# Optimization experiments

Measured on AMD Instinct MI355X. Metric: run time of the kernel, lower is better.

Reference implementation:

```python
import jax, jax.numpy as jnp
import numpy as np

H = 64          # index_n_heads
D = 128         # index_head_dim (== FP8 quant block size -> one scale per row)
RD = 64         # qk_rope_head_dim
TOPK = 512      # index_topk
THETA = 10000.0
SM_SCALE = D ** -0.5


def _fwht(x):
    """Sylvester-ordered fast Walsh-Hadamard transform over last dim, scaled by d^-0.5."""
    d = x.shape[-1]
    orig = x.shape
    y = x.reshape(-1, d)
    m = 1
    while m < d:  # static loop, log2(d)=7 iters
        y = y.reshape(-1, d // (2 * m), 2, m)
        a, b = y[:, :, 0, :], y[:, :, 1, :]
        y = jnp.stack([a + b, a - b], axis=2)
        m *= 2
    return y.reshape(orig) * (d ** -0.5)


def _interleaved_to_half(x):
    # [..., d] with (even, odd) interleaving -> [evens..., odds...]
    return jnp.concatenate([x[..., 0::2], x[..., 1::2]], axis=-1)


def _rope_half(x, cos, sin):
    # x: [..., RD] in half format; cos/sin broadcastable to [..., RD//2]
    x1, x2 = x[..., : RD // 2], x[..., RD // 2:]
    return jnp.concatenate([x1 * cos - x2 * sin, x2 * cos + x1 * sin], axis=-1)


def _layernorm(x, g, b, eps=1e-5):
    mu = jnp.mean(x, axis=-1, keepdims=True)
    var = jnp.mean(jnp.square(x - mu), axis=-1, keepdims=True)
    return (x - mu) * jax.lax.rsqrt(var + eps) * g + b


def _fp8_ue8m0_quant(x2d):
    """Per-row FP8 e4m3 quantization with UE8M0 (power-of-two) scales. x2d: (M, 128)."""
    amax = jnp.maximum(jnp.max(jnp.abs(x2d), axis=1), 1e-4)
    sf = jnp.exp2(jnp.ceil(jnp.log2(amax / 448.0)))               # (M,)
    xq = (x2d * (1.0 / sf)[:, None]).astype(jnp.float8_e4m3fn)
    return xq, sf


def _indexer_fwd(hidden_states, q_lora, positions, wq_b, wk, w_proj, ln_gamma, ln_beta):
    T = hidden_states.shape[0]
    # --- projections ---
    q = (q_lora @ wq_b).reshape(T, H, D)                          # (T,H,D)
    k = _layernorm(hidden_states @ wk, ln_gamma, ln_beta)         # (T,D)
    # --- RoPE on leading RD dims (interleaved -> half, then half rotation) ---
    inv_freq = 1.0 / (THETA ** (jnp.arange(0, RD, 2, dtype=jnp.float32) / RD))  # (RD/2,)
    ang = positions.astype(jnp.float32)[:, None] * inv_freq       # (T,RD/2)
    cos, sin = jnp.cos(ang), jnp.sin(ang)
    q_rot = _rope_half(_interleaved_to_half(q[..., :RD]), cos[:, None, :], sin[:, None, :])
    k_rot = _rope_half(_interleaved_to_half(k[..., :RD]), cos, sin)
    q = jnp.concatenate([q_rot, q[..., RD:]], axis=-1)
    k = jnp.concatenate([k_rot, k[..., RD:]], axis=-1)
    # --- Hadamard rotation ---
    q = _fwht(q)
    k = _fwht(k)
    # --- FP8 UE8M0 quantization (head_dim == quant block -> 1 scale per row) ---
    q_fp8, q_scale = _fp8_ue8m0_quant(q.reshape(T * H, D))
    k_fp8, k_scale = _fp8_ue8m0_quant(k)
    q_scale = q_scale.reshape(T, H)
    # --- gate weights: weights_proj * H^-0.5 * q_scale * softmax_scale ---
    weights = (hidden_states @ w_proj) * (H ** -0.5) * q_scale * SM_SCALE  # (T,H)
    # --- MQA indexer scoring: dequant matmul, ReLU, head-weighted sum ---
    qd = q_fp8.astype(jnp.float32).reshape(T, H, D)
    kd = k_fp8.astype(jnp.float32) * k_scale[:, None]             # (T,D)
    logits = jnp.einsum('thd,sd->ths', qd, kd)                    # (T,H,S)
    scores = jnp.einsum('th,ths->ts', weights, jax.nn.relu(logits))  # (T,S)
    # --- causal mask + top-k token selection ---
    t_idx = jnp.arange(T)
    causal = t_idx[None, :] <= t_idx[:, None]                     # (T,S): s <= t
    scores = jnp.where(causal, scores, jnp.float32(-1e30))
    vals, idx = jax.lax.top_k(scores, TOPK)
    return vals, idx


def setup_inputs() -> dict:
    key = jax.random.key(0)
    ks = jax.random.split(key, 5)
    T, HID, R = 1024, 7168, 1536
    return {
        'hidden_states': jax.random.normal(ks[0], (T, HID), jnp.float32),
        'q_lora': jax.random.normal(ks[1], (T, R), jnp.float32),
        'positions': jnp.arange(T, dtype=jnp.int32),
        'wq_b': jax.random.normal(ks[2], (R, H * D), jnp.float32) * (R ** -0.5),
        'wk': jax.random.normal(ks[3], (HID, D), jnp.float32) * (HID ** -0.5),
        'w_proj': jax.random.normal(ks[4], (HID, H), jnp.float32) * (HID ** -0.5),
        'ln_gamma': jnp.ones((D,), jnp.float32),
        'ln_beta': jnp.zeros((D,), jnp.float32),
    }


def reference(hidden_states, q_lora, positions, wq_b, wk, w_proj, ln_gamma, ln_beta):
    return _indexer_fwd(hidden_states, q_lora, positions, wq_b, wk, w_proj, ln_gamma, ln_beta)
```

## Files before the change

kernel.cpp:

```cpp
#include <hip/hip_runtime.h>
#include <cstdint>
#include <cmath>

#define NT 1024
#define NHID 7168
#define NR 1536
#define NH 64
#define ND 128
#define NTOPK 512
#define TTILE 4
#define KSPLIT 16

typedef float f32x4 __attribute__((ext_vector_type(4)));

__device__ __forceinline__ ushort f2bf(float x) {
  uint32_t u = __float_as_uint(x);
  u += 0x7fffu + ((u >> 16) & 1u);
  return (ushort)(u >> 16);
}
__device__ __forceinline__ float bf2f(ushort u) {
  return __uint_as_float(((uint32_t)u) << 16);
}
__device__ __forceinline__ void gload_lds16(const void* g, void* l) {
  __builtin_amdgcn_global_load_lds(
      (const __attribute__((address_space(1))) uint32_t*)g,
      (__attribute__((address_space(3))) uint32_t*)l, 16, 0, 0);
}
__device__ __forceinline__ uint32_t pk_fp8x4(float a, float b, float c, float d) {
  uint32_t lo = (uint32_t)__builtin_amdgcn_cvt_pk_fp8_f32(a, b, 0, false) & 0xffffu;
  uint32_t hi = (uint32_t)__builtin_amdgcn_cvt_pk_fp8_f32(c, d, 0, false) << 16;
  return lo | hi;
}

__device__ __forceinline__ void rope_fwht_quant(
    float v0, float v1, int l, int pos_t,
    const float* __restrict__ cost, const float* __restrict__ sint,
    uint8_t* __restrict__ out_bytes, float* __restrict__ out_scale) {
  float a = __shfl(v0, (2 * l) & 63, 64);
  float b = __shfl(v0, (2 * l + 1) & 63, 64);
  int fi = l & 31;
  float c = cost[pos_t * 32 + fi];
  float sn = sint[pos_t * 32 + fi];
  float r;
  if (l < 32)
    r = __fsub_rn(__fmul_rn(a, c), __fmul_rn(b, sn));
  else
    r = __fadd_rn(__fmul_rn(b, c), __fmul_rn(a, sn));
  v0 = r;

#pragma unroll
  for (int m = 1; m < 64; m <<= 1) {
    float p0 = __shfl_xor(v0, m, 64);
    float p1 = __shfl_xor(v1, m, 64);
    bool up = (l & m) == 0;
    v0 = up ? __fadd_rn(v0, p0) : __fsub_rn(p0, v0);
    v1 = up ? __fadd_rn(v1, p1) : __fsub_rn(p1, v1);
  }
  {
    float A0 = v0, B0 = v1;
    v0 = __fadd_rn(A0, B0);
    v1 = __fsub_rn(A0, B0);
  }
  const float WS = 0.08838834764831843f;
  v0 = __fmul_rn(v0, WS);
  v1 = __fmul_rn(v1, WS);

  float am = fmaxf(fabsf(v0), fabsf(v1));
#pragma unroll
  for (int m = 1; m < 64; m <<= 1) am = fmaxf(am, __shfl_xor(am, m, 64));
  am = fmaxf(am, 1e-4f);
  float ratio = __fdiv_rn(am, 448.0f);
  uint32_t rb = __float_as_uint(ratio);
  int e = (int)((rb + 0x7fffffu) >> 23) - 127;
  float sf = __uint_as_float((uint32_t)(e + 127) << 23);
  float inv = __uint_as_float((uint32_t)(127 - e) << 23);
  float q0 = __fmul_rn(v0, inv);
  float q1 = __fmul_rn(v1, inv);
  int b0 = __builtin_amdgcn_cvt_pk_fp8_f32(q0, q0, 0, false);
  int b1 = __builtin_amdgcn_cvt_pk_fp8_f32(q1, q1, 0, false);
  out_bytes[l] = (uint8_t)(b0 & 0xff);
  out_bytes[l + 64] = (uint8_t)(b1 & 0xff);
  if (l == 0) *out_scale = sf;
}

__global__ __launch_bounds__(256)
void prep_k(const float* __restrict__ hidden, const float* __restrict__ q_lora,
            const int* __restrict__ pos, uint32_t* __restrict__ hidden8,
            uint32_t* __restrict__ qlora8, float* __restrict__ cost,
            float* __restrict__ sint) {
  int gid = blockIdx.x * 256 + threadIdx.x;
  const int n8h = NT * NHID / 8;
  if (gid < n8h) {
    const f32x4* p = (const f32x4*)(hidden + (size_t)gid * 8);
    f32x4 a = p[0], b = p[1];
    hidden8[(size_t)gid * 2] = pk_fp8x4(a[0], a[1], a[2], a[3]);
    hidden8[(size_t)gid * 2 + 1] = pk_fp8x4(b[0], b[1], b[2], b[3]);
  } else {
    int i = gid - n8h;
    const f32x4* p = (const f32x4*)(q_lora + (size_t)i * 8);
    f32x4 a = p[0], b = p[1];
    qlora8[(size_t)i * 2] = pk_fp8x4(a[0], a[1], a[2], a[3]);
    qlora8[(size_t)i * 2 + 1] = pk_fp8x4(b[0], b[1], b[2], b[3]);
  }
  if (blockIdx.x < NT && threadIdx.x < 32) {
    int t = blockIdx.x, i = threadIdx.x;
    double x = (double)(2 * i) / 64.0;
    double pw = pow(10000.0, x);
    float p32 = (float)pw;
    float invf = __fdiv_rn(1.0f, p32);
    float ang = __fmul_rn((float)pos[t], invf);
    cost[t * 32 + i] = (float)cos((double)ang);
    sint[t * 32 + i] = (float)sin((double)ang);
  }
}

__global__ __launch_bounds__(256)
void tcast_kw_k(const float* __restrict__ wk, const float* __restrict__ wp,
                uint8_t* __restrict__ out) {
  __shared__ uint8_t t8[64][68];
  int tid = threadIdx.x;
  int bx = blockIdx.x;
  const float* in = (bx < 2) ? wk : wp;
  int N = (bx < 2) ? ND : NH;
  int n0 = (bx < 2) ? bx * 64 : 0;
  int orow0 = (bx < 2) ? bx * 64 : 128;
  int k0 = blockIdx.y * 64;
  int r = tid >> 4, c = (tid & 15) * 4;
#pragma unroll
  for (int rr = 0; rr < 64; rr += 16) {
    f32x4 v = *(const f32x4*)(in + (size_t)(k0 + rr + r) * N + n0 + c);
    *(uint32_t*)&t8[rr + r][c] =
        pk_fp8x4(v[0] * 64.0f, v[1] * 64.0f, v[2] * 64.0f, v[3] * 64.0f);
  }
  __syncthreads();
#pragma unroll
  for (int rr = 0; rr < 64; rr += 16) {
    int orow = rr + r;
    uint32_t w = (uint32_t)t8[c + 0][orow] | ((uint32_t)t8[c + 1][orow] << 8) |
                 ((uint32_t)t8[c + 2][orow] << 16) | ((uint32_t)t8[c + 3][orow] << 24);
    *(uint32_t*)(out + (size_t)(orow0 + orow) * NHID + k0 + c) = w;
  }
}

__global__ __launch_bounds__(256)
void tcast_fp8_k(const float* __restrict__ in, uint8_t* __restrict__ out,
                 int K, int N) {
  __shared__ uint8_t t8[64][68];
  int tid = threadIdx.x;
  int n0 = blockIdx.x * 64, k0 = blockIdx.y * 64;
  int r = tid >> 4, c = (tid & 15) * 4;
#pragma unroll
  for (int rr = 0; rr < 64; rr += 16) {
    f32x4 v = *(const f32x4*)(in + (size_t)(k0 + rr + r) * N + n0 + c);
    *(uint32_t*)&t8[rr + r][c] = pk_fp8x4(v[0], v[1], v[2], v[3]);
  }
  __syncthreads();
#pragma unroll
  for (int rr = 0; rr < 64; rr += 16) {
    int orow = rr + r;
    uint32_t w = (uint32_t)t8[c + 0][orow] | ((uint32_t)t8[c + 1][orow] << 8) |
                 ((uint32_t)t8[c + 2][orow] << 16) | ((uint32_t)t8[c + 3][orow] << 24);
    *(uint32_t*)(out + (size_t)(n0 + orow) * K + k0 + c) = w;
  }
}

template <int BM, int BN, bool FUSEQ>
__global__ __launch_bounds__(256)
void gemm_fp8_pipe_k(const uint8_t* __restrict__ A, const uint8_t* __restrict__ Bt,
                     float* __restrict__ C, const float* __restrict__ cost,
                     const float* __restrict__ sint, uint8_t* __restrict__ qfp8,
                     float* __restrict__ qscale, int M, int N, int K, int kchunk) {
  constexpr int FM = BM / 32;
  constexpr int FN = BN / 32;
  constexpr int ABYTES = BM * 64;
  constexpr int BBYTES = BN * 64;
  constexpr int BUF = ABYTES + BBYTES;
  constexpr int LPS = (BM + BN) / 64;
  constexpr int SMEM = FUSEQ ? (128 * 132 * 2) : 2 * BUF;
  __shared__ char smem[SMEM];
  int tid = threadIdx.x;
  int wave = tid >> 6, lane = tid & 63;
  int ln = lane & 15, lg = lane >> 4;
  int n0 = blockIdx.x * BN, m0 = blockIdx.y * BM;
  int k0 = blockIdx.z * kchunk;
  int wm = (wave >> 1) * (BM / 2), wn = (wave & 1) * (BN / 2);

  f32x4 acc[FM][FN];
#pragma unroll
  for (int m = 0; m < FM; m++)
#pragma unroll
    for (int n = 0; n < FN; n++) acc[m][n] = {0.f, 0.f, 0.f, 0.f};

  auto stage = [&](int buf, int kk0) {
    char* base = smem + buf * BUF;
#pragma unroll
    for (int c = 0; c < BM / 64; c++) {
      int o = c * 256 + wave * 64 + lane;
      int row = o >> 2, g = o & 3;
      int gs = g ^ ((row >> 1) & 3);
      gload_lds16(A + (size_t)(m0 + row) * K + kk0 + gs * 16, base + o * 16);
    }
#pragma unroll
    for (int c = 0; c < BN / 64; c++) {
      int o = c * 256 + wave * 64 + lane;
      int row = o >> 2, g = o & 3;
      int gs = g ^ ((row >> 1) & 3);
      gload_lds16(Bt + (size_t)(n0 + row) * K + kk0 + gs * 16,
                  base + ABYTES + o * 16);
    }
  };

  int ntile = kchunk / 64;
  stage(0, k0);
  stage(1, k0 + 64);
  int cur = 0;
  for (int t = 0; t < ntile; t++) {
    if (t < ntile - 1) {
      if constexpr (LPS == 4)
        asm volatile("s_waitcnt vmcnt(4)" ::: "memory");
      else
        asm volatile("s_waitcnt vmcnt(3)" ::: "memory");
    } else {
      asm volatile("s_waitcnt vmcnt(0)" ::: "memory");
    }
    __builtin_amdgcn_s_barrier();
    const uint8_t* ap = (const uint8_t*)smem + cur * BUF;
    const uint8_t* bp = ap + ABYTES;
#pragma unroll
    for (int kk = 0; kk < 2; kk++) {
      long af[FM], bf[FN];
#pragma unroll
      for (int m = 0; m < FM; m++) {
        int row = wm + m * 16 + ln;
        int g = kk * 2 + (lg >> 1);
        af[m] = *(const long*)(ap + row * 64 + ((g ^ ((row >> 1) & 3)) << 4) +
                               (lg & 1) * 8);
      }
#pragma unroll
      for (int n = 0; n < FN; n++) {
        int row = wn + n * 16 + ln;
        int g = kk * 2 + (lg >> 1);
        bf[n] = *(const long*)(bp + row * 64 + ((g ^ ((row >> 1) & 3)) << 4) +
                               (lg & 1) * 8);
      }
#pragma unroll
      for (int m = 0; m < FM; m++)
#pragma unroll
        for (int n = 0; n < FN; n++)
          acc[m][n] = __builtin_amdgcn_mfma_f32_16x16x32_fp8_fp8(af[m], bf[n],
                                                                 acc[m][n], 0, 0, 0);
    }
    __builtin_amdgcn_s_barrier();
    if (t + 2 < ntile) stage(cur, k0 + (t + 2) * 64);
    cur ^= 1;
  }

  if constexpr (FUSEQ) {
    ushort(*qtile)[132] = (ushort(*)[132])smem;
#pragma unroll
    for (int m = 0; m < FM; m++)
#pragma unroll
      for (int n = 0; n < FN; n++)
#pragma unroll
        for (int j = 0; j < 4; j++)
          qtile[wm + m * 16 + lg * 4 + j][wn + n * 16 + ln] = f2bf(acc[m][n][j]);
    __syncthreads();
    int h = blockIdx.x;
    for (int r = 0; r < 32; r++) {
      int row = wave * 32 + r;
      int tq = m0 + row;
      float v0 = bf2f(qtile[row][lane]);
      float v1 = bf2f(qtile[row][64 + lane]);
      rope_fwht_quant(v0, v1, lane, tq, cost, sint,
                      qfp8 + ((size_t)tq * NH + h) * ND,
                      qscale + (size_t)tq * NH + h);
    }
  } else {
    float* Cz = C + (size_t)blockIdx.z * M * N;
#pragma unroll
    for (int m = 0; m < FM; m++)
#pragma unroll
      for (int n = 0; n < FN; n++)
#pragma unroll
        for (int j = 0; j < 4; j++) {
          int row = m0 + wm + m * 16 + lg * 4 + j;
          int col = n0 + wn + n * 16 + ln;
          Cz[(size_t)row * N + col] = acc[m][n][j];
        }
  }
}

__global__ __launch_bounds__(256)
void kfin_weights_k(const float* __restrict__ kpart, const float* __restrict__ gamma,
                    const float* __restrict__ beta, const float* __restrict__ cost,
                    const float* __restrict__ sint, const float* __restrict__ qscale,
                    uint8_t* __restrict__ kfp8, float* __restrict__ kscale,
                    float* __restrict__ weights) {
  int l = threadIdx.x & 63;
  int row = blockIdx.x * 4 + (threadIdx.x >> 6);
  float v0 = 0.0f, v1 = 0.0f, ws = 0.0f;
#pragma unroll
  for (int p = 0; p < KSPLIT; p++) {
    const float* base = kpart + (size_t)p * (NT * 192) + row * 192;
    v0 = __fadd_rn(v0, base[l]);
    v1 = __fadd_rn(v1, base[l + 64]);
    ws = __fadd_rn(ws, base[128 + l]);
  }
  float w = __fmul_rn(ws, 0.001953125f);
  w = __fmul_rn(w, qscale[row * NH + l]);
  w = __fmul_rn(w, 0.08838834764831843f);
  weights[row * NH + l] = w;
  float s = __fadd_rn(v0, v1);
#pragma unroll
  for (int m = 1; m < 64; m <<= 1) s = __fadd_rn(s, __shfl_xor(s, m, 64));
  float mu = __fmul_rn(s, 0.0078125f);
  float d0 = __fsub_rn(v0, mu), d1 = __fsub_rn(v1, mu);
  float vs = __fadd_rn(__fmul_rn(d0, d0), __fmul_rn(d1, d1));
#pragma unroll
  for (int m = 1; m < 64; m <<= 1) vs = __fadd_rn(vs, __shfl_xor(vs, m, 64));
  float var = __fmul_rn(vs, 0.0078125f);
  float rs = (float)(1.0 / sqrt((double)__fadd_rn(var, 1e-5f)));
  v0 = __fadd_rn(__fmul_rn(__fmul_rn(d0, rs), gamma[l]), beta[l]);
  v1 = __fadd_rn(__fmul_rn(__fmul_rn(d1, rs), gamma[l + 64]), beta[l + 64]);
  rope_fwht_quant(v0, v1, l, row, cost, sint, kfp8 + (size_t)row * ND, kscale + row);
}

__global__ __launch_bounds__(256)
void scores_k(const uint8_t* __restrict__ qfp8, const uint8_t* __restrict__ kfp8,
              const float* __restrict__ weights, float* __restrict__ scores) {
  __shared__ uint8_t q_lds[TTILE * 64 * 128];
  __shared__ uint8_t k_lds[128 * 128];
  __shared__ float w_lds[TTILE * 64];

  int b = blockIdx.x;
  int g = 0;
  while (g < 7 && b >= 16 * (g + 1) * (g + 2)) g++;
  int r = b - 16 * g * (g + 1);
  int a = 32 * g + r / (g + 1);
  int chunk = r % (g + 1);
  int t0 = a * TTILE;
  int s0 = chunk * 128;

  int tid = threadIdx.x;
  int wave = tid >> 6, lane = tid & 63;
  int lg = lane >> 4, ln = lane & 15;

  const uint8_t* qbase = qfp8 + (size_t)t0 * 64 * 128;
#pragma unroll
  for (int it = 0; it < 8; it++) {
    int o = it * 256 + wave * 64 + lane;
    int row = o >> 3, G = o & 7;
    int src = row * 128 + ((G ^ ((row >> 1) & 7)) << 4);
    gload_lds16(qbase + src, q_lds + (it * 256 + wave * 64) * 16);
  }
  const uint8_t* kbase = kfp8 + (size_t)s0 * 128;
#pragma unroll
  for (int it = 0; it < 4; it++) {
    int o = it * 256 + wave * 64 + lane;
    int row = o >> 3, G = o & 7;
    int src = row * 128 + ((G ^ ((row >> 1) & 7)) << 4);
    gload_lds16(kbase + src, k_lds + (it * 256 + wave * 64) * 16);
  }
  w_lds[tid] = weights[t0 * NH + tid];
  __syncthreads();

  long bfr[2][4];
#pragma unroll
  for (int sj = 0; sj < 2; sj++) {
    int srow = wave * 32 + sj * 16 + ln;
    int base = srow * 128;
    int xr = ((srow >> 1) & 7) << 4;
#pragma unroll
    for (int ks = 0; ks < 4; ks++)
      bfr[sj][ks] = *(const long*)(k_lds + base + ((ks * 32 + lg * 8) ^ xr));
  }

  float p[TTILE][2];
#pragma unroll
  for (int tt = 0; tt < TTILE; tt++) p[tt][0] = p[tt][1] = 0.0f;

#pragma unroll
  for (int ht = 0; ht < 4; ht++) {
    long afr[TTILE][4];
#pragma unroll
    for (int tt = 0; tt < TTILE; tt++) {
      int qrow = tt * 64 + ht * 16 + ln;
      int base = qrow * 128;
      int xr = ((qrow >> 1) & 7) << 4;
#pragma unroll
      for (int ks = 0; ks < 4; ks++)
        afr[tt][ks] = *(const long*)(q_lds + base + ((ks * 32 + lg * 8) ^ xr));
    }
#pragma unroll
    for (int tt = 0; tt < TTILE; tt++) {
      float wj[4];
#pragma unroll
      for (int j = 0; j < 4; j++) wj[j] = w_lds[tt * 64 + ht * 16 + lg * 4 + j];
#pragma unroll
      for (int sj = 0; sj < 2; sj++) {
        f32x4 acc = {0.f, 0.f, 0.f, 0.f};
#pragma unroll
        for (int ks = 0; ks < 4; ks++)
          acc = __builtin_amdgcn_mfma_f32_16x16x32_fp8_fp8(afr[tt][ks], bfr[sj][ks],
                                                           acc, 0, 0, 0);
#pragma unroll
        for (int j = 0; j < 4; j++)
          p[tt][sj] = fmaf(wj[j], fmaxf(acc[j], 0.0f), p[tt][sj]);
      }
    }
  }

#pragma unroll
  for (int tt = 0; tt < TTILE; tt++)
#pragma unroll
    for (int sj = 0; sj < 2; sj++) {
      float v = p[tt][sj];
      v += __shfl_xor(v, 16, 64);
      v += __shfl_xor(v, 32, 64);
      if (lg == 0)
        scores[(size_t)(t0 + tt) * NT + s0 + wave * 32 + sj * 16 + ln] = v;
    }
}

__global__ __launch_bounds__(256)
void topk_k(const float* __restrict__ scores, const float* __restrict__ kscale,
            float* __restrict__ outv, float* __restrict__ outi) {
  __shared__ unsigned long long key[1024];
  int t = blockIdx.x, tid = threadIdx.x;
#pragma unroll
  for (int p = 0; p < 4; p++) {
    int s = tid + p * 256;
    float v;
    if (s <= t) {
      v = __fmul_rn(scores[(size_t)t * NT + s], kscale[s]);
    } else {
      v = -1e30f;
    }
    unsigned u = __float_as_uint(v);
    unsigned ou = (u & 0x80000000u) ? ~u : (u | 0x80000000u);
    key[s] = ((unsigned long long)ou << 32) | (unsigned)(~(unsigned)s);
  }
  for (int k = 2; k <= 1024; k <<= 1) {
    for (int j = k >> 1; j > 0; j >>= 1) {
      __syncthreads();
#pragma unroll
      for (int p = 0; p < 2; p++) {
        int i = tid + p * 256;
        int l = ((i & ~(j - 1)) << 1) | (i & (j - 1));
        int m = l + j;
        bool desc = ((l & k) == 0);
        unsigned long long a = key[l], b = key[m];
        if (desc ? (a < b) : (a > b)) {
          key[l] = b;
          key[m] = a;
        }
      }
    }
  }
  __syncthreads();
#pragma unroll
  for (int p = 0; p < 2; p++) {
    int r = tid + p * 256;
    unsigned long long kk = key[r];
    unsigned ou = (unsigned)(kk >> 32);
    unsigned u = (ou & 0x80000000u) ? (ou ^ 0x80000000u) : ~ou;
    unsigned idx = (~(unsigned)(kk & 0xffffffffu)) & 1023u;
    outv[(size_t)t * NTOPK + r] = __uint_as_float(u);
    outi[(size_t)t * NTOPK + r] = (float)idx;
  }
}

extern "C" void kernel_launch(void* const* d_in, const int* in_sizes, int n_in,
                              void* d_out, int out_size, void* d_ws, size_t ws_size,
                              hipStream_t stream) {
  const float* hidden = (const float*)d_in[0];
  const float* q_lora = (const float*)d_in[1];
  const int* positions = (const int*)d_in[2];
  const float* wq_b = (const float*)d_in[3];
  const float* wk = (const float*)d_in[4];
  const float* w_proj = (const float*)d_in[5];
  const float* ln_g = (const float*)d_in[6];
  const float* ln_b = (const float*)d_in[7];
  float* out = (float*)d_out;

  char* u0 = (char*)d_ws;
  uint8_t* hidden8 = (uint8_t*)u0;
  uint8_t* wkp8 = (uint8_t*)(u0 + 7340032);
  uint8_t* wqb8 = (uint8_t*)u0;
  uint8_t* qlora8 = (uint8_t*)(u0 + 12582912);
  float* scores = (float*)u0;
  char* p = u0 + 14680064;
  float* kpart = (float*)p;    p += 12582912;
  float* cost = (float*)p;     p += 131072;
  float* sint = (float*)p;     p += 131072;
  float* kscale = (float*)p;   p += 4096;
  float* qscale = (float*)p;   p += 262144;
  float* weights = (float*)p;  p += 262144;
  uint8_t* kfp8 = (uint8_t*)p; p += 131072;
  uint8_t* qfp8 = (uint8_t*)p; p += 8388608;

  prep_k<<<(NT * NHID / 8 + NT * NR / 8) / 256, 256, 0, stream>>>(
      hidden, q_lora, positions, (uint32_t*)hidden8, (uint32_t*)qlora8,
      cost, sint);

  tcast_kw_k<<<dim3(3, 112), 256, 0, stream>>>(wk, w_proj, wkp8);
  gemm_fp8_pipe_k<128, 64, false><<<dim3(3, 8, KSPLIT), 256, 0, stream>>>(
      hidden8, wkp8, kpart, nullptr, nullptr, nullptr, nullptr,
      NT, 192, NHID, NHID / KSPLIT);

  tcast_fp8_k<<<dim3(128, 24), 256, 0, stream>>>(wq_b, wqb8, NR, NH * ND);
  gemm_fp8_pipe_k<128, 128, true><<<dim3(64, 8, 1), 256, 0, stream>>>(
      qlora8, wqb8, nullptr, cost, sint, qfp8, qscale,
      NT, NH * ND, NR, NR);

  kfin_weights_k<<<NT / 4, 256, 0, stream>>>(kpart, ln_g, ln_b, cost, sint,
                                             qscale, kfp8, kscale, weights);

  scores_k<<<1152, 256, 0, stream>>>(qfp8, kfp8, weights, scores);
  topk_k<<<NT, 256, 0, stream>>>(scores, kscale, out, out + (size_t)NT * NTOPK);
}
```

Before: 128.5 us.

## Merge prep and transpose-cast kernels, pre-permute K layout, shrink GEMM tiles

Merges the activation cast, RoPE table and both weight transpose-casts into one prep kernel, which removes two launches. The fp8 outputs are written in a K-permuted order so the GEMM can load 16-byte vectors from LDS without the XOR swizzle. The GEMM drops from 128-row to 64-row tiles, giving more blocks, and replaces the two-deep vmcnt pipeline with a simpler single-prefetch loop synchronised by __syncthreads. The workspace is rearranged so wqb8 and qlora8 no longer alias hidden8. Possible costs are LDS bank conflicts without the swizzle and less latency hiding in the simpler pipeline.

Result: faster. 115.4 us (-10.2%).

```diff
diff --git a/kernel.cpp b/kernel.cpp
--- a/kernel.cpp
+++ b/kernel.cpp
@@ -12,6 +12,7 @@
 #define KSPLIT 16
 
 typedef float f32x4 __attribute__((ext_vector_type(4)));
+typedef long lx2 __attribute__((ext_vector_type(2)));
 
 __device__ __forceinline__ ushort f2bf(float x) {
   uint32_t u = __float_as_uint(x);
@@ -31,6 +32,7 @@
   uint32_t hi = (uint32_t)__builtin_amdgcn_cvt_pk_fp8_f32(c, d, 0, false) << 16;
   return lo | hi;
 }
+
 
 __device__ __forceinline__ void rope_fwht_quant(
     float v0, float v1, int l, int pos_t,
@@ -84,99 +86,96 @@
 }
 
 __global__ __launch_bounds__(256)
-void prep_k(const float* __restrict__ hidden, const float* __restrict__ q_lora,
-            const int* __restrict__ pos, uint32_t* __restrict__ hidden8,
-            uint32_t* __restrict__ qlora8, float* __restrict__ cost,
-            float* __restrict__ sint) {
-  int gid = blockIdx.x * 256 + threadIdx.x;
-  const int n8h = NT * NHID / 8;
-  if (gid < n8h) {
-    const f32x4* p = (const f32x4*)(hidden + (size_t)gid * 8);
-    f32x4 a = p[0], b = p[1];
-    hidden8[(size_t)gid * 2] = pk_fp8x4(a[0], a[1], a[2], a[3]);
-    hidden8[(size_t)gid * 2 + 1] = pk_fp8x4(b[0], b[1], b[2], b[3]);
+void prep_all_k(const float* __restrict__ hidden, const float* __restrict__ q_lora,
+                const float* __restrict__ wk, const float* __restrict__ wp,
+                const float* __restrict__ wq_b, const int* __restrict__ pos,
+                uint32_t* __restrict__ hidden8, uint32_t* __restrict__ qlora8,
+                uint8_t* __restrict__ wkp8, uint8_t* __restrict__ wqb8,
+                float* __restrict__ cost, float* __restrict__ sint) {
+  __shared__ uint8_t t8[64][68];
+  int bid = blockIdx.x, tid = threadIdx.x;
+  if (bid < 4352) {
+    bool isq = bid >= 3584;
+    size_t i = (size_t)(isq ? bid - 3584 : bid) * 256 + tid;
+    const float* src = isq ? q_lora : hidden;
+    uint32_t* dst = isq ? qlora8 : hidden8;
+    const f32x4* pp = (const f32x4*)(src + i * 8);
+    f32x4 a = pp[0], b = pp[1];
+    size_t blk = i >> 3;
+    int j = (int)(i & 7);
+    size_t dw = blk * 16 + (size_t)((j & 3) * 4 + (j >> 2) * 2);
+    dst[dw] = pk_fp8x4(a[0], a[1], a[2], a[3]);
+    dst[dw + 1] = pk_fp8x4(b[0], b[1], b[2], b[3]);
+    if (bid < NT && tid < 32) {
+      int t = bid, ii = tid;
+      double x = (double)(2 * ii) / 64.0;
+      double pw = pow(10000.0, x);
+      float p32 = (float)pw;
+      float invf = __fdiv_rn(1.0f, p32);
+      float ang = __fmul_rn((float)pos[t], invf);
+      cost[t * 32 + ii] = (float)cos((double)ang);
+      sint[t * 32 + ii] = (float)sin((double)ang);
+    }
+    return;
+  }
+  const float* in;
+  uint8_t* out;
+  int N_, n0, orow0, Kdim, k0;
+  float scale;
+  if (bid < 4688) {
+    int local = bid - 4352;
+    int bx = local % 3, by = local / 3;
+    in = (bx < 2) ? wk : wp;
+    N_ = (bx < 2) ? ND : NH;
+    n0 = (bx < 2) ? bx * 64 : 0;
+    orow0 = (bx < 2) ? bx * 64 : 128;
+    Kdim = NHID;
+    k0 = by * 64;
+    out = wkp8;
+    scale = 64.0f;
   } else {
-    int i = gid - n8h;
-    const f32x4* p = (const f32x4*)(q_lora + (size_t)i * 8);
-    f32x4 a = p[0], b = p[1];
-    qlora8[(size_t)i * 2] = pk_fp8x4(a[0], a[1], a[2], a[3]);
-    qlora8[(size_t)i * 2 + 1] = pk_fp8x4(b[0], b[1], b[2], b[3]);
-  }
-  if (blockIdx.x < NT && threadIdx.x < 32) {
-    int t = blockIdx.x, i = threadIdx.x;
-    double x = (double)(2 * i) / 64.0;
-    double pw = pow(10000.0, x);
-    float p32 = (float)pw;
-    float invf = __fdiv_rn(1.0f, p32);
-    float ang = __fmul_rn((float)pos[t], invf);
-    cost[t * 32 + i] = (float)cos((double)ang);
-    sint[t * 32 + i] = (float)sin((double)ang);
-  }
-}
-
-__global__ __launch_bounds__(256)
-void tcast_kw_k(const float* __restrict__ wk, const float* __restrict__ wp,
-                uint8_t* __restrict__ out) {
-  __shared__ uint8_t t8[64][68];
-  int tid = threadIdx.x;
-  int bx = blockIdx.x;
-  const float* in = (bx < 2) ? wk : wp;
-  int N = (bx < 2) ? ND : NH;
-  int n0 = (bx < 2) ? bx * 64 : 0;
-  int orow0 = (bx < 2) ? bx * 64 : 128;
-  int k0 = blockIdx.y * 64;
+    int local = bid - 4688;
+    int nx = local % 128, ky = local / 128;
+    in = wq_b;
+    N_ = NH * ND;
+    n0 = nx * 64;
+    orow0 = n0;
+    Kdim = NR;
+    k0 = ky * 64;
+    out = wqb8;
+    scale = 1.0f;
+  }
   int r = tid >> 4, c = (tid & 15) * 4;
 #pragma unroll
   for (int rr = 0; rr < 64; rr += 16) {
-    f32x4 v = *(const f32x4*)(in + (size_t)(k0 + rr + r) * N + n0 + c);
+    f32x4 v = *(const f32x4*)(in + (size_t)(k0 + rr + r) * N_ + n0 + c);
     *(uint32_t*)&t8[rr + r][c] =
-        pk_fp8x4(v[0] * 64.0f, v[1] * 64.0f, v[2] * 64.0f, v[3] * 64.0f);
+        pk_fp8x4(v[0] * scale, v[1] * scale, v[2] * scale, v[3] * scale);
   }
   __syncthreads();
+  int sp = ((c >> 3) & 3) * 16 + (c >> 5) * 8 + ((c >> 2) & 1) * 4;
 #pragma unroll
   for (int rr = 0; rr < 64; rr += 16) {
     int orow = rr + r;
     uint32_t w = (uint32_t)t8[c + 0][orow] | ((uint32_t)t8[c + 1][orow] << 8) |
                  ((uint32_t)t8[c + 2][orow] << 16) | ((uint32_t)t8[c + 3][orow] << 24);
-    *(uint32_t*)(out + (size_t)(orow0 + orow) * NHID + k0 + c) = w;
-  }
-}
-
-__global__ __launch_bounds__(256)
-void tcast_fp8_k(const float* __restrict__ in, uint8_t* __restrict__ out,
-                 int K, int N) {
-  __shared__ uint8_t t8[64][68];
-  int tid = threadIdx.x;
-  int n0 = blockIdx.x * 64, k0 = blockIdx.y * 64;
-  int r = tid >> 4, c = (tid & 15) * 4;
-#pragma unroll
-  for (int rr = 0; rr < 64; rr += 16) {
-    f32x4 v = *(const f32x4*)(in + (size_t)(k0 + rr + r) * N + n0 + c);
-    *(uint32_t*)&t8[rr + r][c] = pk_fp8x4(v[0], v[1], v[2], v[3]);
-  }
-  __syncthreads();
-#pragma unroll
-  for (int rr = 0; rr < 64; rr += 16) {
-    int orow = rr + r;
-    uint32_t w = (uint32_t)t8[c + 0][orow] | ((uint32_t)t8[c + 1][orow] << 8) |
-                 ((uint32_t)t8[c + 2][orow] << 16) | ((uint32_t)t8[c + 3][orow] << 24);
-    *(uint32_t*)(out + (size_t)(n0 + orow) * K + k0 + c) = w;
+    *(uint32_t*)(out + (size_t)(orow0 + orow) * Kdim + k0 + sp) = w;
   }
 }
 
 template <int BM, int BN, bool FUSEQ>
 __global__ __launch_bounds__(256)
-void gemm_fp8_pipe_k(const uint8_t* __restrict__ A, const uint8_t* __restrict__ Bt,
-                     float* __restrict__ C, const float* __restrict__ cost,
-                     const float* __restrict__ sint, uint8_t* __restrict__ qfp8,
-                     float* __restrict__ qscale, int M, int N, int K, int kchunk) {
+void gemm_fp8_k(const uint8_t* __restrict__ A, const uint8_t* __restrict__ Bt,
+                float* __restrict__ C, const float* __restrict__ cost,
+                const float* __restrict__ sint, uint8_t* __restrict__ qfp8,
+                float* __restrict__ qscale, int M, int N, int K, int kchunk) {
   constexpr int FM = BM / 32;
   constexpr int FN = BN / 32;
   constexpr int ABYTES = BM * 64;
   constexpr int BBYTES = BN * 64;
   constexpr int BUF = ABYTES + BBYTES;
-  constexpr int LPS = (BM + BN) / 64;
-  constexpr int SMEM = FUSEQ ? (128 * 132 * 2) : 2 * BUF;
+  constexpr int OVER = FUSEQ ? BM * 132 * 2 : 0;
+  constexpr int SMEM = (OVER > 2 * BUF) ? OVER : 2 * BUF;
   __shared__ char smem[SMEM];
   int tid = threadIdx.x;
   int wave = tid >> 6, lane = tid & 63;
@@ -195,63 +194,46 @@
     char* base = smem + buf * BUF;
 #pragma unroll
     for (int c = 0; c < BM / 64; c++) {
-      int o = c * 256 + wave * 64 + lane;
-      int row = o >> 2, g = o & 3;
-      int gs = g ^ ((row >> 1) & 3);
-      gload_lds16(A + (size_t)(m0 + row) * K + kk0 + gs * 16, base + o * 16);
+      int o = c * 256 + tid;
+      gload_lds16(A + (size_t)(m0 + (o >> 2)) * K + kk0 + (o & 3) * 16,
+                  base + o * 16);
     }
 #pragma unroll
     for (int c = 0; c < BN / 64; c++) {
-      int o = c * 256 + wave * 64 + lane;
-      int row = o >> 2, g = o & 3;
-      int gs = g ^ ((row >> 1) & 3);
-      gload_lds16(Bt + (size_t)(n0 + row) * K + kk0 + gs * 16,
+      int o = c * 256 + tid;
+      gload_lds16(Bt + (size_t)(n0 + (o >> 2)) * K + kk0 + (o & 3) * 16,
                   base + ABYTES + o * 16);
     }
   };
 
   int ntile = kchunk / 64;
   stage(0, k0);
-  stage(1, k0 + 64);
+  __syncthreads();
   int cur = 0;
   for (int t = 0; t < ntile; t++) {
-    if (t < ntile - 1) {
-      if constexpr (LPS == 4)
-        asm volatile("s_waitcnt vmcnt(4)" ::: "memory");
-      else
-        asm volatile("s_waitcnt vmcnt(3)" ::: "memory");
-    } else {
-      asm volatile("s_waitcnt vmcnt(0)" ::: "memory");
-    }
-    __builtin_amdgcn_s_barrier();
+    if (t + 1 < ntile) stage(cur ^ 1, k0 + (t + 1) * 64);
     const uint8_t* ap = (const uint8_t*)smem + cur * BUF;
     const uint8_t* bp = ap + ABYTES;
-#pragma unroll
-    for (int kk = 0; kk < 2; kk++) {
-      long af[FM], bf[FN];
-#pragma unroll
-      for (int m = 0; m < FM; m++) {
-        int row = wm + m * 16 + ln;
-        int g = kk * 2 + (lg >> 1);
-        af[m] = *(const long*)(ap + row * 64 + ((g ^ ((row >> 1) & 3)) << 4) +
-                               (lg & 1) * 8);
-      }
-#pragma unroll
-      for (int n = 0; n < FN; n++) {
-        int row = wn + n * 16 + ln;
-        int g = kk * 2 + (lg >> 1);
-        bf[n] = *(const long*)(bp + row * 64 + ((g ^ ((row >> 1) & 3)) << 4) +
-                               (lg & 1) * 8);
-      }
-#pragma unroll
-      for (int m = 0; m < FM; m++)
-#pragma unroll
-        for (int n = 0; n < FN; n++)
-          acc[m][n] = __builtin_amdgcn_mfma_f32_16x16x32_fp8_fp8(af[m], bf[n],
-                                                                 acc[m][n], 0, 0, 0);
-    }
-    __builtin_amdgcn_s_barrier();
-    if (t + 2 < ntile) stage(cur, k0 + (t + 2) * 64);
+    lx2 av[FM], bv[FN];
+#pragma unroll
+    for (int m = 0; m < FM; m++)
+      av[m] = *(const lx2*)(ap + (wm + m * 16 + ln) * 64 + lg * 16);
+#pragma unroll
+    for (int n = 0; n < FN; n++)
+      bv[n] = *(const lx2*)(bp + (wn + n * 16 + ln) * 64 + lg * 16);
+#pragma unroll
+    for (int m = 0; m < FM; m++)
+#pragma unroll
+      for (int n = 0; n < FN; n++)
+        acc[m][n] = __builtin_amdgcn_mfma_f32_16x16x32_fp8_fp8(
+            av[m][0], bv[n][0], acc[m][n], 0, 0, 0);
+#pragma unroll
+    for (int m = 0; m < FM; m++)
+#pragma unroll
+      for (int n = 0; n < FN; n++)
+        acc[m][n] = __builtin_amdgcn_mfma_f32_16x16x32_fp8_fp8(
+            av[m][1], bv[n][1], acc[m][n], 0, 0, 0);
+    __syncthreads();
     cur ^= 1;
   }
 
@@ -266,8 +248,8 @@
           qtile[wm + m * 16 + lg * 4 + j][wn + n * 16 + ln] = f2bf(acc[m][n][j]);
     __syncthreads();
     int h = blockIdx.x;
-    for (int r = 0; r < 32; r++) {
-      int row = wave * 32 + r;
+    for (int r = 0; r < BM / 4; r++) {
+      int row = wave * (BM / 4) + r;
       int tq = m0 + row;
       float v0 = bf2f(qtile[row][lane]);
       float v1 = bf2f(qtile[row][64 + lane]);
@@ -486,10 +468,10 @@
   char* u0 = (char*)d_ws;
   uint8_t* hidden8 = (uint8_t*)u0;
   uint8_t* wkp8 = (uint8_t*)(u0 + 7340032);
-  uint8_t* wqb8 = (uint8_t*)u0;
-  uint8_t* qlora8 = (uint8_t*)(u0 + 12582912);
+  uint8_t* wqb8 = (uint8_t*)(u0 + 8716288);
+  uint8_t* qlora8 = (uint8_t*)(u0 + 21299200);
   float* scores = (float*)u0;
-  char* p = u0 + 14680064;
+  char* p = u0 + 22872064;
   float* kpart = (float*)p;    p += 12582912;
   float* cost = (float*)p;     p += 131072;
   float* sint = (float*)p;     p += 131072;
@@ -499,17 +481,16 @@
   uint8_t* kfp8 = (uint8_t*)p; p += 131072;
   uint8_t* qfp8 = (uint8_t*)p; p += 8388608;
 
-  prep_k<<<(NT * NHID / 8 + NT * NR / 8) / 256, 256, 0, stream>>>(
-      hidden, q_lora, positions, (uint32_t*)hidden8, (uint32_t*)qlora8,
-      cost, sint);
-
-  tcast_kw_k<<<dim3(3, 112), 256, 0, stream>>>(wk, w_proj, wkp8);
-  gemm_fp8_pipe_k<128, 64, false><<<dim3(3, 8, KSPLIT), 256, 0, stream>>>(
+  prep_all_k<<<7760, 256, 0, stream>>>(hidden, q_lora, wk, w_proj, wq_b,
+                                       positions, (uint32_t*)hidden8,
+                                       (uint32_t*)qlora8, wkp8, wqb8,
+                                       cost, sint);
+
+  gemm_fp8_k<64, 64, false><<<dim3(3, 16, KSPLIT), 256, 0, stream>>>(
       hidden8, wkp8, kpart, nullptr, nullptr, nullptr, nullptr,
       NT, 192, NHID, NHID / KSPLIT);
 
-  tcast_fp8_k<<<dim3(128, 24), 256, 0, stream>>>(wq_b, wqb8, NR, NH * ND);
-  gemm_fp8_pipe_k<128, 128, true><<<dim3(64, 8, 1), 256, 0, stream>>>(
+  gemm_fp8_k<64, 128, true><<<dim3(64, 16, 1), 256, 0, stream>>>(
       qlora8, wqb8, nullptr, cost, sint, qfp8, qscale,
       NT, NH * ND, NR, NR);
 
```
